# Kernel optimization log

Hardware: AMD Instinct MI355X
Metric: run time of the kernel (lower is better)

The kernel has to match this reference:

```python
import jax, jax.numpy as jnp
import numpy as np

B, S, E, F, R, T = 2, 2048, 768, 3072, 4, 128
H = 12  # num_heads
HD = E // H
HID = 128  # lora_mlp_dim


def _lin(key, out_f, in_f):
    bound = 1.0 / np.sqrt(in_f)
    return jax.random.uniform(key, (out_f, in_f), jnp.float32, -bound, bound)


def _bias(key, out_f, in_f):
    bound = 1.0 / np.sqrt(in_f)
    return jax.random.uniform(key, (out_f,), jnp.float32, -bound, bound)


def setup_inputs() -> dict:
    key = jax.random.key(0)
    ks = jax.random.split(key, 20)
    return {
        "src": jax.random.normal(ks[0], (B, S, E), jnp.float32),
        "task_embedding": jax.random.normal(ks[1], (B, S, T), jnp.float32),
        "norm1_w": jnp.ones((E,), jnp.float32),
        "norm2_w": jnp.ones((E,), jnp.float32),
        "in_proj_w": _lin(ks[2], 3 * E, E),      # MHA qkv, bias=False
        "out_proj_w": _lin(ks[3], E, E),          # MHA out, bias=False
        "ffn1_w": _lin(ks[4], F, E), "ffn1_b": _bias(ks[5], F, E),
        "ffn2_w": _lin(ks[6], E, F), "ffn2_b": _bias(ks[7], E, F),
        "hA_w1": _lin(ks[8], HID, T), "hA_b1": _bias(ks[9], HID, T),
        "hA_w2": _lin(ks[10], F * R, HID), "hA_b2": _bias(ks[11], F * R, HID),
        "hB_w1": _lin(ks[12], HID, T), "hB_b1": _bias(ks[13], HID, T),
        "hB_w2": _lin(ks[14], R * E, HID), "hB_b2": _bias(ks[15], R * E, HID),
    }


def _rmsnorm(x, w):
    eps = jnp.finfo(x.dtype).eps
    return x * jax.lax.rsqrt(jnp.mean(x * x, axis=-1, keepdims=True) + eps) * w


def reference(src, task_embedding, norm1_w, norm2_w, in_proj_w, out_proj_w,
              ffn1_w, ffn1_b, ffn2_w, ffn2_b,
              hA_w1, hA_b1, hA_w2, hA_b2, hB_w1, hB_b1, hB_w2, hB_b2):
    # --- self-attention block (pre-RMSNorm) ---
    x = _rmsnorm(src, norm1_w)
    qkv = jnp.einsum('bse,fe->bsf', x, in_proj_w)  # [B,S,3E]
    q, k, v = jnp.split(qkv, 3, axis=-1)
    q = q.reshape(B, S, H, HD).transpose(0, 2, 1, 3)
    k = k.reshape(B, S, H, HD).transpose(0, 2, 1, 3)
    v = v.reshape(B, S, H, HD).transpose(0, 2, 1, 3)
    scores = jnp.einsum('bhqd,bhkd->bhqk', q, k) / jnp.sqrt(jnp.float32(HD))
    attn = jax.nn.softmax(scores, axis=-1)
    ctx = jnp.einsum('bhqk,bhkd->bhqd', attn, v)
    ctx = ctx.transpose(0, 2, 1, 3).reshape(B, S, E)
    attn_out = jnp.einsum('bse,fe->bsf', ctx, out_proj_w)
    src = src + attn_out

    # --- FFN block with per-token hypernetwork LoRA on linear1 ---
    x = _rmsnorm(src, norm2_w)
    # hypernetwork: MLP(task) -> per-token A [F,R], B [R,E]
    hA = jax.nn.relu(jnp.einsum('bst,ht->bsh', task_embedding, hA_w1) + hA_b1)
    A_params = (jnp.einsum('bsh,fh->bsf', hA, hA_w2) + hA_b2).reshape(B, S, F, R)
    hB = jax.nn.relu(jnp.einsum('bst,ht->bsh', task_embedding, hB_w1) + hB_b1)
    B_params = (jnp.einsum('bsh,fh->bsf', hB, hB_w2) + hB_b2).reshape(B, S, R, E)

    base = jnp.einsum('bse,fe->bsf', x, ffn1_w) + ffn1_b  # [B,S,F]
    inter = jnp.einsum('bse,bsre->bsr', x, B_params)       # [B,S,R]
    adapt = jnp.einsum('bsr,bsfr->bsf', inter, A_params)   # [B,S,F]
    h = jax.nn.relu(base + adapt)
    out2 = jnp.einsum('bsf,ef->bse', h, ffn2_w) + ffn2_b
    return src + out2
```

## Files before the change

### kernel.cpp

```cpp
#include <hip/hip_runtime.h>
#include <math.h>

#define NB 2
#define NS 2048
#define NE 768
#define NF 3072
#define NHEAD 12
#define NTOK 4096
#define LDW 1344

typedef __bf16 bf16;
typedef __bf16 bf16x4 __attribute__((ext_vector_type(4)));
typedef __bf16 bf16x8 __attribute__((ext_vector_type(8)));
typedef float  f32x4  __attribute__((ext_vector_type(4)));

__device__ __forceinline__ f32x4 mfma_bf16(bf16x8 a, bf16x8 b, f32x4 c) {
  return __builtin_amdgcn_mfma_f32_16x16x32_bf16(a, b, c, 0, 0, 0);
}

__device__ __forceinline__ float fast_exp2(float x) {
#if __has_builtin(__builtin_amdgcn_exp2f)
  return __builtin_amdgcn_exp2f(x);
#else
  return exp2f(x);
#endif
}

__device__ __forceinline__ void glds16(const void* g, void* l) {
  __builtin_amdgcn_global_load_lds((const __attribute__((address_space(1))) void*)g,
                                   (__attribute__((address_space(3))) void*)l,
                                   16, 0, 0);
}

__device__ __forceinline__ void swz_xy(int& bx, int& by) {
  int gx = gridDim.x;
  int i = by*gx + bx;
  int xcd = i & 7, s = i >> 3;
  int bands = gridDim.y >> 3;
  by = xcd*bands + s / gx;
  bx = s % gx;
}

__global__ void prep_kernel(const float* __restrict__ in_proj, const float* __restrict__ out_proj,
                            const float* __restrict__ ffn1_w, const float* __restrict__ ffn1_b,
                            const float* __restrict__ ffn2_w,
                            const float* __restrict__ hA_w1, const float* __restrict__ hA_b1,
                            const float* __restrict__ hA_w2, const float* __restrict__ hA_b2,
                            const float* __restrict__ hB_w1, const float* __restrict__ hB_b1,
                            const float* __restrict__ hB_w2,
                            const float* __restrict__ task,
                            bf16* __restrict__ Wqkv, bf16* __restrict__ Wo, bf16* __restrict__ W2,
                            bf16* __restrict__ W1ab, float* __restrict__ b1ab,
                            bf16* __restrict__ WBp, bf16* __restrict__ Wc,
                            bf16* __restrict__ task_bf)
{
  __shared__ float tb[64*130];
  int stride = gridDim.x * blockDim.x;
  int t0 = blockIdx.x * blockDim.x + threadIdx.x;
  const float QS = 0.125f * 1.44269504088896f;
  for (int i = t0; i < (2304*768)/4; i += stride) {
    float4 v = ((const float4*)in_proj)[i];
    float sc = (i < (768*768)/4) ? QS : 1.0f;
    *(bf16x4*)(Wqkv + i*4) = (bf16x4){(bf16)(v.x*sc), (bf16)(v.y*sc), (bf16)(v.z*sc), (bf16)(v.w*sc)};
  }
  for (int i = t0; i < (768*768)/4; i += stride) {
    float4 v = ((const float4*)out_proj)[i];
    *(bf16x4*)(Wo + i*4) = (bf16x4){(bf16)v.x, (bf16)v.y, (bf16)v.z, (bf16)v.w};
  }
  for (int i = t0; i < (768*3072)/4; i += stride) {
    float4 v = ((const float4*)ffn2_w)[i];
    *(bf16x4*)(W2 + i*4) = (bf16x4){(bf16)v.x, (bf16)v.y, (bf16)v.z, (bf16)v.w};
  }
  for (int i = t0; i < (NTOK*128)/4; i += stride) {
    float4 v = ((const float4*)task)[i];
    *(bf16x4*)(task_bf + i*4) = (bf16x4){(bf16)v.x, (bf16)v.y, (bf16)v.z, (bf16)v.w};
  }
  for (int i = t0; i < 256*128;  i += stride)
    W1ab[i] = (bf16)(i < 128*128 ? hA_w1[i] : hB_w1[i - 128*128]);
  for (int i = t0; i < 256; i += stride) b1ab[i] = (i < 128) ? hA_b1[i] : hB_b1[i-128];

  for (int j0 = blockIdx.x*64; j0 < 3072; j0 += gridDim.x*64) {
    __syncthreads();
    for (int i = threadIdx.x; i < 64*128; i += 256) {
      int jr = i >> 7, hh = i & 127;
      tb[jr*130 + hh] = hB_w2[(long)(j0 + jr)*128 + hh];
    }
    __syncthreads();
    int r = j0 / 768, e0 = j0 % 768;
    for (int i = threadIdx.x; i < 128*64; i += 256) {
      int hh = i >> 6, jr = i & 63;
      WBp[(long)(r*128 + hh)*768 + e0 + jr] = (bf16)tb[jr*130 + hh];
    }
  }

  for (int f = blockIdx.x; f < 3072; f += gridDim.x) {
    const float* hrow = hA_w2 + (long)f*512;
    bf16* wrow = Wc + (long)f*LDW;
    for (int c = threadIdx.x; c < 768; c += 256) wrow[c] = (bf16)ffn1_w[(long)f*768 + c];
    for (int i = threadIdx.x; i < 512; i += 256) {
      int r = i >> 7, h = i & 127;
      wrow[768 + h*4 + r] = (bf16)hrow[i];
    }
    if (threadIdx.x < 4)        wrow[1280 + threadIdx.x] = (bf16)hA_b2[f*4 + threadIdx.x];
    else if (threadIdx.x == 4)  wrow[1284] = (bf16)ffn1_b[f];
    else if (threadIdx.x < 64)  wrow[1280 + threadIdx.x] = (bf16)0.f;
  }
}

__global__ __launch_bounds__(256) void rmsnorm_k(const float* __restrict__ x,
                                                 const float* __restrict__ w,
                                                 bf16* __restrict__ out, int ld_out)
{
  __shared__ float red[4];
  long t = blockIdx.x;
  const float* xr = x + t*NE;
  float ss = 0.f;
  #pragma unroll
  for (int i = 0; i < 3; i++) { float v = xr[threadIdx.x + i*256]; ss += v*v; }
  #pragma unroll
  for (int d = 1; d < 64; d <<= 1) ss += __shfl_xor(ss, d, 64);
  if ((threadIdx.x & 63) == 0) red[threadIdx.x >> 6] = ss;
  __syncthreads();
  float tot = red[0] + red[1] + red[2] + red[3];
  float scale = rsqrtf(tot * (1.f/768.f) + 1.1920928955078125e-07f);
  #pragma unroll
  for (int i = 0; i < 3; i++) {
    int idx = threadIdx.x + i*256;
    out[t*ld_out + idx] = (bf16)(xr[idx] * scale * w[idx]);
  }
}

template<typename OutT, bool RELU, bool BIAS, bool RES>
__global__ __launch_bounds__(256) void gemm_bt_sw(const bf16* __restrict__ A,
                                                  const bf16* __restrict__ Bm,
                                                  OutT* __restrict__ C,
                                                  const float* __restrict__ bias,
                                                  const float* __restrict__ res,
                                                  int K, int lda, int ldb, int ldc)
{
  __shared__ bf16 As[2][128*32];
  __shared__ bf16 Bs[2][128*32];
  const int tid = threadIdx.x;
  int bx = blockIdx.x, by = blockIdx.y;
  swz_xy(bx, by);
  const int m0 = by * 128;
  const int n0 = bx * 128;
  const int w = tid >> 6, lane = tid & 63;
  const int quad = lane >> 4, l16 = lane & 15;
  const int wy = w >> 1, wx = w & 1;

  f32x4 acc[4][4];
  #pragma unroll
  for (int i = 0; i < 4; i++)
    #pragma unroll
    for (int j = 0; j < 4; j++) acc[i][j] = (f32x4){0.f,0.f,0.f,0.f};

  const int i0 = tid, i1 = tid + 256;
  const int R0 = i0 >> 3, cc0 = (i0 & 7) ^ (R0 & 7), r0 = 2*R0 + (cc0 >> 2), ch0 = (cc0 & 3) * 8;
  const int R1 = i1 >> 3, cc1 = (i1 & 7) ^ (R1 & 7), r1 = 2*R1 + (cc1 >> 2), ch1 = (cc1 & 3) * 8;
  const bf16* pA0 = A  + (long)(m0 + r0)*lda + ch0;
  const bf16* pA1 = A  + (long)(m0 + r1)*lda + ch1;
  const bf16* pB0 = Bm + (long)(n0 + r0)*ldb + ch0;
  const bf16* pB1 = Bm + (long)(n0 + r1)*ldb + ch1;
  auto stage = [&](int buf) {
    glds16(pA0, (void*)(&As[buf][i0*8]));
    glds16(pA1, (void*)(&As[buf][i1*8]));
    glds16(pB0, (void*)(&Bs[buf][i0*8]));
    glds16(pB1, (void*)(&Bs[buf][i1*8]));
    pA0 += 32; pA1 += 32; pB0 += 32; pB1 += 32;
  };

  stage(0);
  __builtin_amdgcn_s_waitcnt(0);
  __syncthreads();

  const int Rh = l16 >> 1;
  const int ppq = ((l16 & 1) << 2) | quad;
  const int jfr = ppq ^ Rh;
  const int nsteps = K >> 5;
  for (int s = 0; s < nsteps; ++s) {
    const int cur = s & 1;
    if (s + 1 < nsteps) stage(cur ^ 1);

    bf16x8 af[4], bfr[4];
    #pragma unroll
    for (int mi = 0; mi < 4; ++mi)
      af[mi] = *(const bf16x8*)(&As[cur][(wy*32 + mi*8 + Rh)*64 + jfr*8]);
    #pragma unroll
    for (int ni = 0; ni < 4; ++ni)
      bfr[ni] = *(const bf16x8*)(&Bs[cur][(wx*32 + ni*8 + Rh)*64 + jfr*8]);
    #pragma unroll
    for (int mi = 0; mi < 4; ++mi)
      #pragma unroll
      for (int ni = 0; ni < 4; ++ni)
        acc[mi][ni] = mfma_bf16(af[mi], bfr[ni], acc[mi][ni]);

    __builtin_amdgcn_s_waitcnt(0);
    __syncthreads();
  }

  #pragma unroll
  for (int mi = 0; mi < 4; ++mi)
    #pragma unroll
    for (int ni = 0; ni < 4; ++ni) {
      int col = n0 + wx*64 + ni*16 + l16;
      #pragma unroll
      for (int r = 0; r < 4; ++r) {
        long row = m0 + wy*64 + mi*16 + quad*4 + r;
        float v = acc[mi][ni][r];
        if (BIAS) v += bias[col];
        if (RES)  v += res[row*ldc + col];
        if (RELU) v = v > 0.f ? v : 0.f;
        C[row*ldc + col] = (OutT)v;
      }
    }
}

template<typename OutT, bool RELU, bool BIAS, bool RES>
__global__ __launch_bounds__(256) void gemm64(const bf16* __restrict__ A,
                                              const bf16* __restrict__ Bm,
                                              OutT* __restrict__ C,
                                              const float* __restrict__ bias,
                                              const float* __restrict__ res,
                                              int K, int lda, int ldb, int ldc)
{
  __shared__ bf16 As[2][64*64];
  __shared__ bf16 Bs[2][64*64];
  const int tid = threadIdx.x;
  int bx = blockIdx.x, by = blockIdx.y;
  swz_xy(bx, by);
  const int m0 = by * 64, n0 = bx * 64;
  const int w = tid >> 6, lane = tid & 63;
  const int quad = lane >> 4, l16 = lane & 15;
  const int wy = w >> 1, wx = w & 1;
  const int sw = l16 & 7;

  f32x4 acc[2][2];
  #pragma unroll
  for (int i = 0; i < 2; i++)
    #pragma unroll
    for (int j = 0; j < 2; j++) acc[i][j] = (f32x4){0.f,0.f,0.f,0.f};

  const int c0 = tid, c1 = tid + 256;
  const int r0 = c0 >> 3, g0 = ((c0 & 7) ^ (r0 & 7)) * 8;
  const int r1 = c1 >> 3, g1 = ((c1 & 7) ^ (r1 & 7)) * 8;
  const bf16* pA0 = A  + (long)(m0 + r0)*lda + g0;
  const bf16* pA1 = A  + (long)(m0 + r1)*lda + g1;
  const bf16* pB0 = Bm + (long)(n0 + r0)*ldb + g0;
  const bf16* pB1 = Bm + (long)(n0 + r1)*ldb + g1;
  auto stage = [&](int buf) {
    glds16(pA0, (void*)(&As[buf][c0*8]));
    glds16(pA1, (void*)(&As[buf][c1*8]));
    glds16(pB0, (void*)(&Bs[buf][c0*8]));
    glds16(pB1, (void*)(&Bs[buf][c1*8]));
    pA0 += 64; pA1 += 64; pB0 += 64; pB1 += 64;
  };

  stage(0);
  __builtin_amdgcn_s_waitcnt(0);
  __syncthreads();

  const int nsteps = K >> 6;
  for (int s = 0; s < nsteps; ++s) {
    const int cur = s & 1;
    if (s + 1 < nsteps) stage(cur ^ 1);

    bf16x8 af[2][2], bfr[2][2];
    #pragma unroll
    for (int mi = 0; mi < 2; ++mi)
      #pragma unroll
      for (int kb = 0; kb < 2; ++kb)
        af[mi][kb] = *(const bf16x8*)(&As[cur][(wy*32 + mi*16 + l16)*64 + (((kb*4 + quad) ^ sw))*8]);
    #pragma unroll
    for (int ni = 0; ni < 2; ++ni)
      #pragma unroll
      for (int kb = 0; kb < 2; ++kb)
        bfr[ni][kb] = *(const bf16x8*)(&Bs[cur][(wx*32 + ni*16 + l16)*64 + (((kb*4 + quad) ^ sw))*8]);
    #pragma unroll
    for (int kb = 0; kb < 2; ++kb)
      #pragma unroll
      for (int mi = 0; mi < 2; ++mi)
        #pragma unroll
        for (int ni = 0; ni < 2; ++ni)
          acc[mi][ni] = mfma_bf16(af[mi][kb], bfr[ni][kb], acc[mi][ni]);

    __builtin_amdgcn_s_waitcnt(0);
    __syncthreads();
  }

  #pragma unroll
  for (int mi = 0; mi < 2; ++mi)
    #pragma unroll
    for (int ni = 0; ni < 2; ++ni) {
      int col = n0 + wx*32 + ni*16 + l16;
      #pragma unroll
      for (int r = 0; r < 4; ++r) {
        long row = m0 + wy*32 + mi*16 + quad*4 + r;
        float v = acc[mi][ni][r];
        if (BIAS) v += bias[col];
        if (RES)  v += res[row*ldc + col];
        if (RELU) v = v > 0.f ? v : 0.f;
        C[row*ldc + col] = (OutT)v;
      }
    }
}

__global__ __launch_bounds__(256) void gemm_qkv64(const bf16* __restrict__ A,
                                                  const bf16* __restrict__ Bm,
                                                  bf16* __restrict__ Qkv,
                                                  bf16* __restrict__ Vt)
{
  __shared__ bf16 As[2][64*64];
  __shared__ bf16 Bs[2][64*64];
  const int tid = threadIdx.x;
  int bx = blockIdx.x, by = blockIdx.y;
  swz_xy(bx, by);
  const int m0 = by * 64, n0 = bx * 64;
  const int w = tid >> 6, lane = tid & 63;
  const int quad = lane >> 4, l16 = lane & 15;
  const int wy = w >> 1, wx = w & 1;
  const int sw = l16 & 7;

  f32x4 acc[2][2];
  #pragma unroll
  for (int i = 0; i < 2; i++)
    #pragma unroll
    for (int j = 0; j < 2; j++) acc[i][j] = (f32x4){0.f,0.f,0.f,0.f};

  const int c0 = tid, c1 = tid + 256;
  const int r0 = c0 >> 3, g0 = ((c0 & 7) ^ (r0 & 7)) * 8;
  const int r1 = c1 >> 3, g1 = ((c1 & 7) ^ (r1 & 7)) * 8;
  const bf16* pA0 = A  + (long)(m0 + r0)*768 + g0;
  const bf16* pA1 = A  + (long)(m0 + r1)*768 + g1;
  const bf16* pB0 = Bm + (long)(n0 + r0)*768 + g0;
  const bf16* pB1 = Bm + (long)(n0 + r1)*768 + g1;
  auto stage = [&](int buf) {
    glds16(pA0, (void*)(&As[buf][c0*8]));
    glds16(pA1, (void*)(&As[buf][c1*8]));
    glds16(pB0, (void*)(&Bs[buf][c0*8]));
    glds16(pB1, (void*)(&Bs[buf][c1*8]));
    pA0 += 64; pA1 += 64; pB0 += 64; pB1 += 64;
  };

  stage(0);
  __builtin_amdgcn_s_waitcnt(0);
  __syncthreads();

  for (int s = 0; s < 12; ++s) {
    const int cur = s & 1;
    if (s + 1 < 12) stage(cur ^ 1);

    bf16x8 af[2][2], bfr[2][2];
    #pragma unroll
    for (int mi = 0; mi < 2; ++mi)
      #pragma unroll
      for (int kb = 0; kb < 2; ++kb)
        af[mi][kb] = *(const bf16x8*)(&As[cur][(wy*32 + mi*16 + l16)*64 + (((kb*4 + quad) ^ sw))*8]);
    #pragma unroll
    for (int ni = 0; ni < 2; ++ni)
      #pragma unroll
      for (int kb = 0; kb < 2; ++kb)
        bfr[ni][kb] = *(const bf16x8*)(&Bs[cur][(wx*32 + ni*16 + l16)*64 + (((kb*4 + quad) ^ sw))*8]);
    #pragma unroll
    for (int kb = 0; kb < 2; ++kb)
      #pragma unroll
      for (int mi = 0; mi < 2; ++mi)
        #pragma unroll
        for (int ni = 0; ni < 2; ++ni)
          acc[mi][ni] = mfma_bf16(af[mi][kb], bfr[ni][kb], acc[mi][ni]);

    __builtin_amdgcn_s_waitcnt(0);
    __syncthreads();
  }

  const int bb = m0 >> 11;
  #pragma unroll
  for (int mi = 0; mi < 2; ++mi)
    #pragma unroll
    for (int ni = 0; ni < 2; ++ni) {
      int col = n0 + wx*32 + ni*16 + l16;
      #pragma unroll
      for (int r = 0; r < 4; ++r) {
        long row = m0 + wy*32 + mi*16 + quad*4 + r;
        bf16 v = (bf16)acc[mi][ni][r];
        if (col < 1536) {
          Qkv[row*2304 + col] = v;
        } else {
          int vc = col - 1536;
          int hh = vc >> 6, d = vc & 63;
          long srow = row & (NS-1);
          Vt[((long)(bb*NHEAD + hh)*64 + d)*NS + srow] = v;
        }
      }
    }
}

__global__ __launch_bounds__(256, 3) void flash_attn(const bf16* __restrict__ Qkv,
                                                     const bf16* __restrict__ Vt,
                                                     bf16* __restrict__ Ctx)
{
  __shared__ bf16 Ks[2][2][64*64];

  const int tid = threadIdx.x;
  const int w = tid >> 6, lane = tid & 63;
  const int quad = lane >> 4, l16 = lane & 15;
  const int pair = w >> 1, qw = w & 1;
  int bx = blockIdx.x, by = blockIdx.y;
  swz_xy(bx, by);
  const int bh = by;
  const int b = bh / NHEAD, h = bh % NHEAD;
  const int q0 = bx * 64;

  bf16x8 qf[2][2];
  #pragma unroll
  for (int mi = 0; mi < 2; ++mi) {
    const long tq = (long)(b*NS + q0 + qw*32 + mi*16 + l16);
    qf[mi][0] = *(const bf16x8*)(Qkv + tq*2304 + h*64 + quad*8);
    qf[mi][1] = *(const bf16x8*)(Qkv + tq*2304 + h*64 + 32 + quad*8);
  }

  bf16x8 ones;
  #pragma unroll
  for (int j = 0; j < 8; ++j) ones[j] = (bf16)1.0f;

  f32x4 o[2][4];
  f32x4 o5[2];
  #pragma unroll
  for (int mi = 0; mi < 2; ++mi) {
    o5[mi] = (f32x4){0.f,0.f,0.f,0.f};
    #pragma unroll
    for (int i = 0; i < 4; i++) o[mi][i] = (f32x4){0.f,0.f,0.f,0.f};
  }

  const int ptid = tid & 127;
  const bf16* kp[4];
  int cc[4];
  #pragma unroll
  for (int i = 0; i < 4; ++i) {
    int c = ptid + i*128;
    cc[i] = c;
    int r = c >> 3, g = ((c & 7) ^ (r & 7)) * 8;
    kp[i] = Qkv + (long)(b*NS + pair*1024 + r)*2304 + 768 + h*64 + g;
  }
  auto stage = [&](int buf) {
    #pragma unroll
    for (int i = 0; i < 4; ++i) {
      glds16(kp[i], (void*)(&Ks[pair][buf][cc[i]*8]));
      kp[i] += (long)64*2304;
    }
  };

  const bf16* vB = Vt + ((long)bh*64 + l16)*NS + pair*1024 + quad*8;

  auto body = [&](int cur) {
    bf16x8 vf0[4];
    #pragma unroll
    for (int dt = 0; dt < 4; ++dt)
      vf0[dt] = *(const bf16x8*)(vB + (long)dt*16*NS);

    bf16x8 kfr[4][2];
    #pragma unroll
    for (int nt = 0; nt < 4; ++nt)
      #pragma unroll
      for (int kb = 0; kb < 2; ++kb)
        kfr[nt][kb] = *(const bf16x8*)(&Ks[pair][cur][(nt*16 + l16)*64 + (((kb*4 + quad) ^ (l16 & 7)))*8]);

    bf16x8 pf[2][2];
    #pragma unroll
    for (int mi = 0; mi < 2; ++mi) {
      f32x4 s[4];
      #pragma unroll
      for (int nt = 0; nt < 4; ++nt) {
        s[nt] = (f32x4){0.f,0.f,0.f,0.f};
        #pragma unroll
        for (int kb = 0; kb < 2; ++kb)
          s[nt] = mfma_bf16(kfr[nt][kb], qf[mi][kb], s[nt]);
      }
      #pragma unroll
      for (int nt = 0; nt < 4; ++nt)
        #pragma unroll
        for (int r = 0; r < 4; ++r)
          pf[mi][nt >> 1][(nt & 1)*4 + r] = (bf16)fast_exp2(s[nt][r]);
    }

    bf16x8 vf1[4];
    #pragma unroll
    for (int dt = 0; dt < 4; ++dt)
      vf1[dt] = *(const bf16x8*)(vB + (long)dt*16*NS + 32);
    vB += 64;

    #pragma unroll
    for (int mi = 0; mi < 2; ++mi) {
      #pragma unroll
      for (int dt = 0; dt < 4; ++dt)
        o[mi][dt] = mfma_bf16(pf[mi][0], vf0[dt], o[mi][dt]);
      o5[mi] = mfma_bf16(pf[mi][0], ones, o5[mi]);
    }
    #pragma unroll
    for (int mi = 0; mi < 2; ++mi) {
      #pragma unroll
      for (int dt = 0; dt < 4; ++dt)
        o[mi][dt] = mfma_bf16(pf[mi][1], vf1[dt], o[mi][dt]);
      o5[mi] = mfma_bf16(pf[mi][1], ones, o5[mi]);
    }
  };

  stage(0);
  __builtin_amdgcn_s_waitcnt(0);
  __syncthreads();

  for (int t = 0; t < 16; t += 2) {
    stage(1);
    body(0);
    __builtin_amdgcn_s_waitcnt(0);
    __syncthreads();
    if (t + 2 < 16) stage(0);
    body(1);
    __builtin_amdgcn_s_waitcnt(0);
    __syncthreads();
  }

  float* Of = (float*)&Ks[0][0][0];
  float* Lf = Of + 64*68;
  const int rbase = qw*32;
  if (pair == 1) {
    #pragma unroll
    for (int mi = 0; mi < 2; ++mi)
      #pragma unroll
      for (int r = 0; r < 4; ++r) {
        int row = rbase + mi*16 + quad*4 + r;
        if (l16 == 0) Lf[row] = o5[mi][r];
        #pragma unroll
        for (int dt = 0; dt < 4; ++dt)
          Of[row*68 + dt*16 + l16] = o[mi][dt][r];
      }
  }
  __syncthreads();
  if (pair == 0) {
    #pragma unroll
    for (int mi = 0; mi < 2; ++mi)
      #pragma unroll
      for (int r = 0; r < 4; ++r) {
        int row = rbase + mi*16 + quad*4 + r;
        float inv = 1.f / (o5[mi][r] + Lf[row]);
        long trow = (long)(b*NS + q0 + row);
        #pragma unroll
        for (int dt = 0; dt < 4; ++dt)
          Ctx[trow*NE + h*64 + dt*16 + l16] =
            (bf16)((o[mi][dt][r] + Of[row*68 + dt*16 + l16]) * inv);
      }
  }
}

__global__ __launch_bounds__(256) void build_g(const bf16* __restrict__ HAB,
                                               const float* __restrict__ P,
                                               const float* __restrict__ hB_b2,
                                               bf16* __restrict__ Aext)
{
  long t = blockIdx.x*4 + (threadIdx.x >> 6);
  int lane = threadIdx.x & 63;
  const bf16* xr = Aext + t*LDW;
  float acc[4] = {0.f, 0.f, 0.f, 0.f};
  for (int i = lane; i < 768; i += 64) {
    float xv = (float)xr[i];
    #pragma unroll
    for (int r = 0; r < 4; ++r) acc[r] += xv * hB_b2[r*768 + i];
  }
  const bf16* hB = HAB + t*256 + 128;
  const float* Pr = P + t*512;
  #pragma unroll
  for (int k = 0; k < 2; ++k) {
    int h = lane + k*64;
    float hv = (float)hB[h];
    #pragma unroll
    for (int r = 0; r < 4; ++r) acc[r] += hv * Pr[r*128 + h];
  }
  #pragma unroll
  for (int r = 0; r < 4; ++r)
    #pragma unroll
    for (int d = 1; d < 64; d <<= 1) acc[r] += __shfl_xor(acc[r], d, 64);

  bf16* grow = Aext + t*LDW + 768;
  const bf16* hA = HAB + t*256;
  #pragma unroll
  for (int j = 0; j < 8; ++j) {
    int idx = lane*8 + j;
    int h = idx >> 2, r = idx & 3;
    grow[idx] = (bf16)((float)hA[h] * acc[r]);
  }
  if (lane < 4)       Aext[t*LDW + 1280 + lane] = (bf16)acc[lane];
  else if (lane == 4) Aext[t*LDW + 1284] = (bf16)1.0f;
  else                Aext[t*LDW + 1280 + lane] = (bf16)0.f;
}

extern "C" void kernel_launch(void* const* d_in, const int* in_sizes, int n_in,
                              void* d_out, int out_size, void* d_ws, size_t ws_size,
                              hipStream_t stream)
{
  const float* src      = (const float*)d_in[0];
  const float* task     = (const float*)d_in[1];
  const float* norm1_w  = (const float*)d_in[2];
  const float* norm2_w  = (const float*)d_in[3];
  const float* in_proj  = (const float*)d_in[4];
  const float* out_proj = (const float*)d_in[5];
  const float* ffn1_w   = (const float*)d_in[6];
  const float* ffn1_b   = (const float*)d_in[7];
  const float* ffn2_w   = (const float*)d_in[8];
  const float* ffn2_b   = (const float*)d_in[9];
  const float* hA_w1    = (const float*)d_in[10];
  const float* hA_b1    = (const float*)d_in[11];
  const float* hA_w2    = (const float*)d_in[12];
  const float* hA_b2    = (const float*)d_in[13];
  const float* hB_w1    = (const float*)d_in[14];
  const float* hB_b1    = (const float*)d_in[15];
  const float* hB_w2    = (const float*)d_in[16];
  const float* hB_b2    = (const float*)d_in[17];
  float* out = (float*)d_out;

  char* ws = (char*)d_ws;
  size_t off = 0;
  auto alloc = [&](size_t bytes) { size_t o = off; off += (bytes + 255) & ~(size_t)255; return o; };
  bf16*  Wqkv   = (bf16*)(ws + alloc(2304*768*2));
  bf16*  Wo     = (bf16*)(ws + alloc(768*768*2));
  bf16*  W2     = (bf16*)(ws + alloc(768*3072*2));
  bf16*  W1ab   = (bf16*)(ws + alloc(256*128*2));
  float* b1ab   = (float*)(ws + alloc(256*4));
  bf16*  WBp    = (bf16*)(ws + alloc(512*768*2));
  bf16*  Wc     = (bf16*)(ws + alloc((size_t)3072*LDW*2));
  bf16*  taskbf = (bf16*)(ws + alloc((size_t)NTOK*128*2));
  bf16*  XC     = (bf16*)(ws + alloc((size_t)NTOK*768*2));
  char*  QKVH   = ws + alloc(25165824);
  bf16*  Qkv    = (bf16*)QKVH;
  bf16*  Vt     = (bf16*)(QKVH + 18874368);
  bf16*  Hbuf   = (bf16*)QKVH;
  float* Src2   = (float*)(ws + alloc((size_t)NTOK*768*4));
  bf16*  Aext   = (bf16*)(ws + alloc((size_t)NTOK*LDW*2));
  bf16*  HAB    = (bf16*)(ws + alloc((size_t)NTOK*256*2));
  float* P      = (float*)(ws + alloc((size_t)NTOK*512*4));

  prep_kernel<<<dim3(1280), 256, 0, stream>>>(in_proj, out_proj, ffn1_w, ffn1_b, ffn2_w,
      hA_w1, hA_b1, hA_w2, hA_b2, hB_w1, hB_b1, hB_w2, task,
      Wqkv, Wo, W2, W1ab, b1ab, WBp, Wc, taskbf);
  rmsnorm_k<<<dim3(NTOK), 256, 0, stream>>>(src, norm1_w, XC, 768);
  gemm_qkv64<<<dim3(36,64), 256, 0, stream>>>(XC, Wqkv, Qkv, Vt);
  flash_attn<<<dim3(32,24), 256, 0, stream>>>(Qkv, Vt, XC);
  gemm64<float,false,false,true><<<dim3(12,64), 256, 0, stream>>>(XC, Wo, Src2, nullptr, src, 768, 768, 768, 768);
  rmsnorm_k<<<dim3(NTOK), 256, 0, stream>>>(Src2, norm2_w, Aext, LDW);
  gemm64<bf16,true,true,false><<<dim3(4,64), 256, 0, stream>>>(taskbf, W1ab, HAB, b1ab, nullptr, 128, 128, 128, 256);
  gemm64<float,false,false,false><<<dim3(8,64), 256, 0, stream>>>(Aext, WBp, P, nullptr, nullptr, 768, LDW, 768, 512);
  build_g<<<dim3(NTOK/4), 256, 0, stream>>>(HAB, P, hB_b2, Aext);
  gemm_bt_sw<bf16,true,false,false><<<dim3(24,32), 256, 0, stream>>>(Aext, Wc, Hbuf, nullptr, nullptr, 1312, LDW, LDW, 3072);
  gemm64<float,false,true,true><<<dim3(12,64), 256, 0, stream>>>(Hbuf, W2, out, ffn2_b, Src2, 3072, 3072, 3072, 768);
}
```

Before: 231.1 us.

## Stage V tiles through LDS with async loads and pad the Vt row stride

The flash attention kernel used to read V fragments straight from global memory in every iteration. It now double-buffers V into shared memory with the same glds16 async staging used for K, and reads swizzled fragments from LDS. The transposed V buffer row stride is padded from 2048 to 2176 elements, likely to avoid channel or bank conflicts, and the workspace grows to match. Shared memory per block doubles, so launch bounds drop from 3 to 2 blocks per CU, which lowers occupancy.

Result: faster. 212.4 us (-8.1%).

```diff
diff --git a/kernel.cpp b/kernel.cpp
--- a/kernel.cpp
+++ b/kernel.cpp
@@ -8,6 +8,7 @@
 #define NHEAD 12
 #define NTOK 4096
 #define LDW 1344
+#define VTS 2176
 
 typedef __bf16 bf16;
 typedef __bf16 bf16x4 __attribute__((ext_vector_type(4)));
@@ -389,17 +390,18 @@
           int vc = col - 1536;
           int hh = vc >> 6, d = vc & 63;
           long srow = row & (NS-1);
-          Vt[((long)(bb*NHEAD + hh)*64 + d)*NS + srow] = v;
+          Vt[((long)(bb*NHEAD + hh)*64 + d)*VTS + srow] = v;
         }
       }
     }
 }
 
-__global__ __launch_bounds__(256, 3) void flash_attn(const bf16* __restrict__ Qkv,
+__global__ __launch_bounds__(256, 2) void flash_attn(const bf16* __restrict__ Qkv,
                                                      const bf16* __restrict__ Vt,
                                                      bf16* __restrict__ Ctx)
 {
   __shared__ bf16 Ks[2][2][64*64];
+  __shared__ bf16 Vs[2][2][64*64];
 
   const int tid = threadIdx.x;
   const int w = tid >> 6, lane = tid & 63;
@@ -434,6 +436,7 @@
 
   const int ptid = tid & 127;
   const bf16* kp[4];
+  const bf16* vp[4];
   int cc[4];
   #pragma unroll
   for (int i = 0; i < 4; ++i) {
@@ -441,23 +444,18 @@
     cc[i] = c;
     int r = c >> 3, g = ((c & 7) ^ (r & 7)) * 8;
     kp[i] = Qkv + (long)(b*NS + pair*1024 + r)*2304 + 768 + h*64 + g;
+    vp[i] = Vt + ((long)bh*64 + r)*VTS + pair*1024 + g;
   }
   auto stage = [&](int buf) {
     #pragma unroll
     for (int i = 0; i < 4; ++i) {
       glds16(kp[i], (void*)(&Ks[pair][buf][cc[i]*8]));
-      kp[i] += (long)64*2304;
+      glds16(vp[i], (void*)(&Vs[pair][buf][cc[i]*8]));
+      kp[i] += (long)64*2304; vp[i] += 64;
     }
   };
 
-  const bf16* vB = Vt + ((long)bh*64 + l16)*NS + pair*1024 + quad*8;
-
   auto body = [&](int cur) {
-    bf16x8 vf0[4];
-    #pragma unroll
-    for (int dt = 0; dt < 4; ++dt)
-      vf0[dt] = *(const bf16x8*)(vB + (long)dt*16*NS);
-
     bf16x8 kfr[4][2];
     #pragma unroll
     for (int nt = 0; nt < 4; ++nt)
@@ -482,26 +480,25 @@
         for (int r = 0; r < 4; ++r)
           pf[mi][nt >> 1][(nt & 1)*4 + r] = (bf16)fast_exp2(s[nt][r]);
     }
-
-    bf16x8 vf1[4];
-    #pragma unroll
-    for (int dt = 0; dt < 4; ++dt)
-      vf1[dt] = *(const bf16x8*)(vB + (long)dt*16*NS + 32);
-    vB += 64;
-
-    #pragma unroll
-    for (int mi = 0; mi < 2; ++mi) {
-      #pragma unroll
-      for (int dt = 0; dt < 4; ++dt)
-        o[mi][dt] = mfma_bf16(pf[mi][0], vf0[dt], o[mi][dt]);
-      o5[mi] = mfma_bf16(pf[mi][0], ones, o5[mi]);
-    }
-    #pragma unroll
-    for (int mi = 0; mi < 2; ++mi) {
-      #pragma unroll
-      for (int dt = 0; dt < 4; ++dt)
-        o[mi][dt] = mfma_bf16(pf[mi][1], vf1[dt], o[mi][dt]);
-      o5[mi] = mfma_bf16(pf[mi][1], ones, o5[mi]);
+    #pragma unroll
+    for (int ntp = 0; ntp < 2; ++ntp) {
+      bf16x8 vf[4];
+      #pragma unroll
+      for (int dt = 0; dt < 4; ++dt) {
+        int row = dt*16 + l16;
+        int cA = ntp*4 + (quad >> 1);
+        int base = row*64 + (quad & 1)*4;
+        bf16x4 va = *(const bf16x4*)(&Vs[pair][cur][base + ((cA       ^ (row & 7)) << 3)]);
+        bf16x4 vb = *(const bf16x4*)(&Vs[pair][cur][base + (((cA + 2) ^ (row & 7)) << 3)]);
+        vf[dt] = (bf16x8){va[0],va[1],va[2],va[3], vb[0],vb[1],vb[2],vb[3]};
+      }
+      #pragma unroll
+      for (int mi = 0; mi < 2; ++mi) {
+        #pragma unroll
+        for (int dt = 0; dt < 4; ++dt)
+          o[mi][dt] = mfma_bf16(pf[mi][ntp], vf[dt], o[mi][dt]);
+        o5[mi] = mfma_bf16(pf[mi][ntp], ones, o5[mi]);
+      }
     }
   };
 
@@ -629,7 +626,7 @@
   bf16*  Wc     = (bf16*)(ws + alloc((size_t)3072*LDW*2));
   bf16*  taskbf = (bf16*)(ws + alloc((size_t)NTOK*128*2));
   bf16*  XC     = (bf16*)(ws + alloc((size_t)NTOK*768*2));
-  char*  QKVH   = ws + alloc(25165824);
+  char*  QKVH   = ws + alloc(25559040);
   bf16*  Qkv    = (bf16*)QKVH;
   bf16*  Vt     = (bf16*)(QKVH + 18874368);
   bf16*  Hbuf   = (bf16*)QKVH;
```
